# Optimization experiments

Hardware: AMD Instinct MI355X
Metric: run time of the kernel (lower is better)

Reference implementation:

```python
import jax, jax.numpy as jnp
import numpy as np

N = 50000   # nodes
E = 800000  # edges
D = 128     # input feature dim
H = 128     # hidden dim
L = 3       # num GIN layers
G = 64      # graphs in batch


def setup_inputs() -> dict:
    key = jax.random.key(0)
    ks = jax.random.split(key, 20)
    inp = {
        "h": jax.random.normal(ks[0], (N, D), jnp.float32),
        "src": jax.random.randint(ks[1], (E,), 0, N),
        "dst": jax.random.randint(ks[2], (E,), 0, N),
        "graph_ids": jnp.sort(jax.random.randint(ks[3], (N,), 0, G)),
    }
    k = 4
    for i in range(L):
        in_dim = D if i == 0 else H
        inp[f"w1_{i}"] = jax.random.normal(ks[k], (in_dim, H), jnp.float32) / np.sqrt(in_dim).astype(np.float32); k += 1
        inp[f"b1_{i}"] = jnp.zeros((H,), jnp.float32)
        inp[f"w2_{i}"] = jax.random.normal(ks[k], (H, H), jnp.float32) / np.sqrt(H).astype(np.float32); k += 1
        inp[f"b2_{i}"] = jnp.zeros((H,), jnp.float32)
    inp["w_out"] = jax.random.normal(ks[k], (H * L, 1), jnp.float32) / np.sqrt(H * L).astype(np.float32)
    inp["b_out"] = jnp.zeros((1,), jnp.float32)
    return inp


def _gin_layer(h, src, dst, w1, b1, w2, b2):
    # sum aggregation over edges: agg[i] = sum_{(j->i) in E} h[j]
    agg = jax.ops.segment_sum(h[src], dst, num_segments=N)
    z = h + agg  # (1 + eps) * h + agg with eps = 0 (DGL GINConv default)
    return jax.nn.relu(z @ w1 + b1) @ w2 + b2  # 2-layer MLP


def reference(h, src, dst, graph_ids,
              w1_0, b1_0, w2_0, b2_0,
              w1_1, b1_1, w2_1, b2_1,
              w1_2, b1_2, w2_2, b2_2,
              w_out, b_out):
    layers = [(w1_0, b1_0, w2_0, b2_0),
              (w1_1, b1_1, w2_1, b2_1),
              (w1_2, b1_2, w2_2, b2_2)]
    readouts = []
    for w1, b1, w2, b2 in layers:
        h = _gin_layer(h, src, dst, w1, b1, w2, b2)
        # per-graph sum readout of node features: [G, H]
        readouts.append(jax.ops.segment_sum(h, graph_ids, num_segments=G))
    hg = jnp.concatenate(readouts, axis=1)  # [G, H*L]
    return hg @ w_out + b_out  # [G, 1]
```

## Files before the change

kernel.cpp:

```cpp
#include <hip/hip_runtime.h>

#define NN 50000
#define NE 800000
#define DIMH 128
#define NGRAPH 64
#define NTILES 3125
#define MLP_BLOCKS 1563
#define NBIN 196
#define BCAP 8064
#define SL_US 800000
#define SL_U4 100000

typedef __attribute__((ext_vector_type(8))) short bf16x8;
typedef __attribute__((ext_vector_type(4))) float f32x4;

__device__ __forceinline__ unsigned short f2b(float f) {
  unsigned int b = __float_as_uint(f);
  unsigned int r = (b + 0x7FFFu + ((b >> 16) & 1u)) >> 16;
  return (unsigned short)r;
}
__device__ __forceinline__ float b2f_lo(unsigned int u) { return __uint_as_float(u << 16); }
__device__ __forceinline__ float b2f_hi(unsigned int u) { return __uint_as_float(u & 0xffff0000u); }
__device__ __forceinline__ unsigned int pk2(float lo, float hi) {
  return (unsigned int)f2b(lo) | ((unsigned int)f2b(hi) << 16);
}
__device__ __forceinline__ void add8(float* a, uint4 u) {
  a[0] += b2f_lo(u.x); a[1] += b2f_hi(u.x);
  a[2] += b2f_lo(u.y); a[3] += b2f_hi(u.y);
  a[4] += b2f_lo(u.z); a[5] += b2f_hi(u.z);
  a[6] += b2f_lo(u.w); a[7] += b2f_hi(u.w);
}


__global__ __launch_bounds__(256) void bin_scatter_kernel(const int* __restrict__ src,
                                                          const int* __restrict__ dst,
                                                          int* __restrict__ gcnt,
                                                          int2* __restrict__ staging) {
  __shared__ int hist[NBIN];
  __shared__ int base[NBIN];
  int tid = threadIdx.x;
  for (int i = tid; i < NBIN; i += 256) hist[i] = 0;
  __syncthreads();
  int e0 = blockIdx.x * 2048;
  int2 ed[8];
  int bin[8], rank[8];
#pragma unroll
  for (int k = 0; k < 8; ++k) {
    int e = e0 + k * 256 + tid;
    bin[k] = 0; rank[k] = 0; ed[k] = make_int2(0, 0);
    if (e < NE) {
      ed[k].x = src[e]; ed[k].y = dst[e];
      bin[k] = ed[k].y >> 8;
      rank[k] = atomicAdd(&hist[bin[k]], 1);
    }
  }
  __syncthreads();
  for (int i = tid; i < NBIN; i += 256) base[i] = atomicAdd(&gcnt[i], hist[i]);
  __syncthreads();
#pragma unroll
  for (int k = 0; k < 8; ++k) {
    int e = e0 + k * 256 + tid;
    if (e < NE) staging[bin[k] * BCAP + base[bin[k]] + rank[k]] = ed[k];
  }
}

__global__ __launch_bounds__(256) void bin_fill_kernel(const int2* __restrict__ staging,
                                                       const int* __restrict__ gcnt,
                                                       int* __restrict__ adj,
                                                       int* __restrict__ row_ptr,
                                                       int* __restrict__ cnt,
                                                       int* __restrict__ alloc) {
  __shared__ int hdeg[256], loc[256], c2[256];
  __shared__ int sbase;
  int b = blockIdx.x;
  int tid = threadIdx.x;
  hdeg[tid] = 0; c2[tid] = 0;
  __syncthreads();
  int n = gcnt[b];
  for (int i = tid; i < n; i += 256)
    atomicAdd(&hdeg[staging[b * BCAP + i].y & 255], 1);
  __syncthreads();
  int v = hdeg[tid];
  int va = (v + 1) & ~1;
  loc[tid] = va;
  __syncthreads();
  for (int off = 1; off < 256; off <<= 1) {
    int t = (tid >= off) ? loc[tid - off] : 0;
    __syncthreads();
    loc[tid] += t;
    __syncthreads();
  }
  if (tid == 255) sbase = atomicAdd(alloc, loc[255]);
  __syncthreads();
  int excl = loc[tid] - va;
  int node = b * 256 + tid;
  if (node < NN) { row_ptr[node] = sbase + excl; cnt[node] = v; }
  loc[tid] = excl;
  __syncthreads();
  for (int i = tid; i < n; i += 256) {
    int2 e = staging[b * BCAP + i];
    int local = e.y & 255;
    int r = atomicAdd(&c2[local], 1);
    adj[sbase + loc[local] + r] = e.x;
  }
}


struct WPtrs { const float* w[6]; const float* b_out; const float* b2_last;
               const float* w_out; };

__global__ __launch_bounds__(256) void prep_kernel(WPtrs ptrs, unsigned short* __restrict__ wt,
                                                   float* __restrict__ out,
                                                   int* __restrict__ gcnt,
                                                   int* __restrict__ alloc,
                                                   float* __restrict__ v2,
                                                   float* __restrict__ s2) {
  int i = blockIdx.x * 256 + threadIdx.x;
  int m = i >> 14;
  int idx = i & 16383;
  int c = idx >> 7, k = idx & 127;
  wt[m * 16384 + idx] = f2b(ptrs.w[m][k * DIMH + c]);
  if (i < NGRAPH) out[i] = ptrs.b_out[0];
  if (i < NBIN) gcnt[i] = 0;
  if (i == NBIN) *alloc = 0;
  if (i < DIMH) {
    const float* w2r = ptrs.w[5] + i * DIMH;
    const float* wo = ptrs.w_out + 2 * DIMH;
    float s0 = 0.f, s1 = 0.f, sa = 0.f, sb = 0.f;
#pragma unroll 4
    for (int cc = 0; cc < DIMH; cc += 4) {
      s0 += w2r[cc] * wo[cc];
      s1 += w2r[cc + 1] * wo[cc + 1];
      sa += w2r[cc + 2] * wo[cc + 2];
      sb += w2r[cc + 3] * wo[cc + 3];
    }
    v2[i] = (s0 + s1) + (sa + sb);
  }
  if (i == DIMH) {
    const float* wo = ptrs.w_out + 2 * DIMH;
    float s0 = 0.f, s1 = 0.f, sa = 0.f, sb = 0.f;
#pragma unroll 4
    for (int cc = 0; cc < DIMH; cc += 4) {
      s0 += ptrs.b2_last[cc] * wo[cc];
      s1 += ptrs.b2_last[cc + 1] * wo[cc + 1];
      sa += ptrs.b2_last[cc + 2] * wo[cc + 2];
      sb += ptrs.b2_last[cc + 3] * wo[cc + 3];
    }
    *s2 = (s0 + s1) + (sa + sb);
  }
}

__global__ void convh_kernel(const float* __restrict__ h, uint2* __restrict__ Hs) {
  int t = blockIdx.x * 256 + threadIdx.x;
  if (t >= NN * 32) return;
  int node = t >> 5;
  int q = t & 31;
  float4 v = *(const float4*)&h[node * DIMH + q * 4];
  uint2 o;
  o.x = pk2(v.x, v.y);
  o.y = pk2(v.z, v.w);
  Hs[(q >> 2) * (SL_U4 * 2) + node * 4 + (q & 3)] = o;
}

__global__ __launch_bounds__(256) void agg_kernel(const uint4* __restrict__ Hs,
                                                  const int* __restrict__ row_ptr,
                                                  const int* __restrict__ cnt,
                                                  const int* __restrict__ adj,
                                                  uint4* __restrict__ Zs) {
  int bid = blockIdx.x;
  int slice = bid & 7;
  int nb = bid >> 3;
  int tid = threadIdx.x;
  int node = nb * 128 + (tid >> 1);
  int l2 = tid & 1;
  if (node >= NN) return;
  const uint4* hp = Hs + slice * SL_U4;
  int start = row_ptr[node];
  int c = cnt[node];
  float a[8];
  {
    uint4 own = hp[node * 2 + l2];
    a[0] = b2f_lo(own.x); a[1] = b2f_hi(own.x);
    a[2] = b2f_lo(own.y); a[3] = b2f_hi(own.y);
    a[4] = b2f_lo(own.z); a[5] = b2f_hi(own.z);
    a[6] = b2f_lo(own.w); a[7] = b2f_hi(own.w);
  }
  int j = 0;
  for (; j + 8 <= c; j += 8) {
    int2 i01 = *(const int2*)(adj + start + j);
    int2 i23 = *(const int2*)(adj + start + j + 2);
    int2 i45 = *(const int2*)(adj + start + j + 4);
    int2 i67 = *(const int2*)(adj + start + j + 6);
    uint4 u0 = hp[i01.x * 2 + l2];
    uint4 u1 = hp[i01.y * 2 + l2];
    uint4 u2 = hp[i23.x * 2 + l2];
    uint4 u3 = hp[i23.y * 2 + l2];
    uint4 u4 = hp[i45.x * 2 + l2];
    uint4 u5 = hp[i45.y * 2 + l2];
    uint4 u6 = hp[i67.x * 2 + l2];
    uint4 u7 = hp[i67.y * 2 + l2];
    add8(a, u0); add8(a, u1); add8(a, u2); add8(a, u3);
    add8(a, u4); add8(a, u5); add8(a, u6); add8(a, u7);
  }
  for (; j + 2 <= c; j += 2) {
    int2 i01 = *(const int2*)(adj + start + j);
    uint4 u0 = hp[i01.x * 2 + l2];
    uint4 u1 = hp[i01.y * 2 + l2];
    add8(a, u0); add8(a, u1);
  }
  if (j < c) {
    int n0 = adj[start + j];
    add8(a, hp[n0 * 2 + l2]);
  }
  uint4 o;
  o.x = pk2(a[0], a[1]);
  o.y = pk2(a[2], a[3]);
  o.z = pk2(a[4], a[5]);
  o.w = pk2(a[6], a[7]);
  Zs[slice * SL_U4 + node * 2 + l2] = o;
}

__global__ __launch_bounds__(256, 4) void mlp_kernel(const unsigned short* __restrict__ X,
                                                     const unsigned short* __restrict__ W1t,
                                                     const float* __restrict__ b1,
                                                     const unsigned short* __restrict__ W2t,
                                                     const float* __restrict__ b2,
                                                     unsigned short* __restrict__ Y,
                                                     const int* __restrict__ gids,
                                                     const float* __restrict__ wout,
                                                     float* __restrict__ gout,
                                                     const float* __restrict__ v2,
                                                     const float* __restrict__ s2p) {
  __shared__ unsigned short y1[2][2048];
  __shared__ float s_gout[NGRAPH];
  int tid = threadIdx.x;
  if (tid < NGRAPH) s_gout[tid] = 0.f;
  bool last = (v2 != nullptr);

  int wv = tid >> 6;
  int lane = tid & 63;
  int pb = wv >> 1;
  int half = wv & 1;
  int l15 = lane & 15;
  int g = lane >> 4;
  int rtc = blockIdx.x * 2 + pb;
  bool active = rtc < NTILES;
  int rts = active ? rtc : 0;

  int asl_base = (g >> 1) * SL_US + (g & 1) * 8 + l15 * 16;
  bf16x8 a[4];
  {
    int roff = rts * 256;
#pragma unroll
    for (int kt = 0; kt < 4; ++kt)
      a[kt] = *(const bf16x8*)(X + 2 * kt * SL_US + roff + asl_base);
  }

  bf16x8 fb1[4][4];
  const unsigned short* w1b = W1t + (half * 64 + l15) * DIMH + g * 8;
#pragma unroll
  for (int n = 0; n < 4; ++n)
#pragma unroll
    for (int kt = 0; kt < 4; ++kt)
      fb1[n][kt] = *(const bf16x8*)(w1b + n * 16 * DIMH + kt * 32);

  float b1v[4], v2v[4];
#pragma unroll
  for (int n = 0; n < 4; ++n) {
    int col = half * 64 + n * 16 + l15;
    b1v[n] = b1[col];
    v2v[n] = last ? v2[col] : 0.f;
  }
  float s2v = last ? *s2p : 0.f;
  __syncthreads();

  unsigned short* buf = y1[pb];
  if (active) {
    float pr1[4] = {0.f, 0.f, 0.f, 0.f};
#pragma unroll
    for (int n = 0; n < 4; ++n) {
      f32x4 acc = (f32x4){0.f, 0.f, 0.f, 0.f};
#pragma unroll
      for (int kt = 0; kt < 4; ++kt)
        acc = __builtin_amdgcn_mfma_f32_16x16x32_bf16(a[kt], fb1[n][kt], acc, 0, 0, 0);
      int col2 = (half * 64 + n * 16 + l15) * 2;
#pragma unroll
      for (int r = 0; r < 4; ++r) {
        float f = fmaxf(acc[r] + b1v[n], 0.f);
        if (!last) {
          int row = 4 * g + r;
          buf[((row * 256 + col2) ^ (row << 4)) >> 1] = f2b(f);
        } else {
          pr1[r] += f * v2v[n];
        }
      }
    }
    if (last) {
#pragma unroll
      for (int r = 0; r < 4; ++r) {
#pragma unroll
        for (int off = 1; off < 16; off <<= 1) pr1[r] += __shfl_xor(pr1[r], off, 64);
      }
      if (l15 == 0) {
        float s2add = (half == 0) ? s2v : 0.f;
#pragma unroll
        for (int r = 0; r < 4; ++r)
          atomicAdd(&s_gout[gids[rtc * 16 + 4 * g + r]], pr1[r] + s2add);
      }
    }
  }

  if (!last) {
    bf16x8 fb2[4][4];
    const unsigned short* w2b = W2t + (half * 64 + l15) * DIMH + g * 8;
#pragma unroll
    for (int n = 0; n < 4; ++n)
#pragma unroll
      for (int kt = 0; kt < 4; ++kt)
        fb2[n][kt] = *(const bf16x8*)(w2b + n * 16 * DIMH + kt * 32);
    float b2v[4], wov[4];
#pragma unroll
    for (int n = 0; n < 4; ++n) {
      int col = half * 64 + n * 16 + l15;
      b2v[n] = b2[col];
      wov[n] = wout[col];
    }

    __syncthreads();

    if (active) {
      bf16x8 a2[4];
#pragma unroll
      for (int kt = 0; kt < 4; ++kt)
        a2[kt] = *(const bf16x8*)&buf[((l15 * 256 + kt * 64 + g * 16) ^ (l15 << 4)) >> 1];

      float pr[4] = {0.f, 0.f, 0.f, 0.f};
#pragma unroll
      for (int n = 0; n < 4; ++n) {
        f32x4 acc = (f32x4){0.f, 0.f, 0.f, 0.f};
#pragma unroll
        for (int kt = 0; kt < 4; ++kt)
          acc = __builtin_amdgcn_mfma_f32_16x16x32_bf16(a2[kt], fb2[n][kt], acc, 0, 0, 0);
        int sl = 4 * half + n;
#pragma unroll
        for (int r = 0; r < 4; ++r) {
          float f = acc[r] + b2v[n];
          Y[sl * SL_US + (rtc * 16 + 4 * g + r) * 16 + l15] = f2b(f);
          pr[r] += f * wov[n];
        }
      }
#pragma unroll
      for (int r = 0; r < 4; ++r) {
#pragma unroll
        for (int off = 1; off < 16; off <<= 1) pr[r] += __shfl_xor(pr[r], off, 64);
      }
      if (l15 == 0) {
#pragma unroll
        for (int r = 0; r < 4; ++r)
          atomicAdd(&s_gout[gids[rtc * 16 + 4 * g + r]], pr[r]);
      }
    }
  }

  __syncthreads();
  if (tid < NGRAPH) {
    float v = s_gout[tid];
    if (v != 0.f) atomicAdd(&gout[tid], v);
  }
}


extern "C" void kernel_launch(void* const* d_in, const int* in_sizes, int n_in,
                              void* d_out, int out_size, void* d_ws, size_t ws_size,
                              hipStream_t stream) {
  const float* h = (const float*)d_in[0];
  const int* src = (const int*)d_in[1];
  const int* dst = (const int*)d_in[2];
  const int* gids = (const int*)d_in[3];
  const float* w_out = (const float*)d_in[16];
  const float* b_out = (const float*)d_in[17];
  float* out = (float*)d_out;

  char* base = (char*)d_ws;
  unsigned short* buf0 = (unsigned short*)(base);
  unsigned short* buf1 = (unsigned short*)(base + 12800000);
  int2* staging = (int2*)(base + 25600000);
  int* adj = (int*)(base + 38400000);
  int* row_ptr = (int*)(base + 41800064);
  int* cnt = (int*)(base + 42000128);
  int* gcnt = (int*)(base + 42200192);
  int* alloc = (int*)(base + 42201024);
  unsigned short* wt = (unsigned short*)(base + 42201088);
  float* v2 = (float*)(base + 42397696);
  float* s2 = (float*)(base + 42398208);
  unsigned short* Zs = (unsigned short*)(base + 42400000);

  WPtrs ptrs;
  for (int l = 0; l < 3; ++l) {
    ptrs.w[2 * l] = (const float*)d_in[4 + l * 4];
    ptrs.w[2 * l + 1] = (const float*)d_in[6 + l * 4];
  }
  ptrs.b_out = b_out;
  ptrs.b2_last = (const float*)d_in[15];
  ptrs.w_out = w_out;

  prep_kernel<<<384, 256, 0, stream>>>(ptrs, wt, out, gcnt, alloc, v2, s2);
  bin_scatter_kernel<<<(NE + 2047) / 2048, 256, 0, stream>>>(src, dst, gcnt, staging);
  bin_fill_kernel<<<NBIN, 256, 0, stream>>>(staging, gcnt, adj, row_ptr, cnt, alloc);
  convh_kernel<<<(NN * 32 + 255) / 256, 256, 0, stream>>>(h, (uint2*)buf0);

  int agg_blocks = 391 * 8;

  for (int l = 0; l < 3; ++l) {
    const float* b1 = (const float*)d_in[5 + l * 4];
    const float* b2 = (const float*)d_in[7 + l * 4];
    const unsigned short* Hl = (l & 1) ? buf1 : buf0;
    unsigned short* Yl = (l & 1) ? buf0 : buf1;
    int lastl = (l == 2);
    agg_kernel<<<agg_blocks, 256, 0, stream>>>((const uint4*)Hl, row_ptr, cnt, adj,
                                               (uint4*)Zs);
    mlp_kernel<<<MLP_BLOCKS, 256, 0, stream>>>(Zs, wt + (2 * l) * 16384, b1,
                                               wt + (2 * l + 1) * 16384, b2,
                                               lastl ? nullptr : Yl,
                                               gids, w_out + l * DIMH, out,
                                               lastl ? v2 : nullptr,
                                               lastl ? s2 : nullptr);
  }
}
```

Measured before the change: 237.0 us.

## Make MLP kernels persistent with weight reuse and next-tile prefetch

```diff
diff --git a/kernel.cpp b/kernel.cpp
--- a/kernel.cpp
+++ b/kernel.cpp
@@ -5,7 +5,9 @@
 #define DIMH 128
 #define NGRAPH 64
 #define NTILES 3125
-#define MLP_BLOCKS 1563
+#define PAIRS 1024
+#define MLP_BLOCKS 512
+#define MLP_ITERS 4
 #define NBIN 196
 #define BCAP 8064
 #define SL_US 800000
@@ -220,22 +222,19 @@
   Zs[slice * SL_U4 + node * 2 + l2] = o;
 }
 
-__global__ __launch_bounds__(256, 4) void mlp_kernel(const unsigned short* __restrict__ X,
-                                                     const unsigned short* __restrict__ W1t,
-                                                     const float* __restrict__ b1,
-                                                     const unsigned short* __restrict__ W2t,
-                                                     const float* __restrict__ b2,
-                                                     unsigned short* __restrict__ Y,
-                                                     const int* __restrict__ gids,
-                                                     const float* __restrict__ wout,
-                                                     float* __restrict__ gout,
-                                                     const float* __restrict__ v2,
-                                                     const float* __restrict__ s2p) {
-  __shared__ unsigned short y1[2][2048];
+__global__ __launch_bounds__(256, 2) void mlp_mid_kernel(const unsigned short* __restrict__ X,
+                                                         const unsigned short* __restrict__ W1t,
+                                                         const float* __restrict__ b1,
+                                                         const unsigned short* __restrict__ W2t,
+                                                         const float* __restrict__ b2,
+                                                         unsigned short* __restrict__ Y,
+                                                         const int* __restrict__ gids,
+                                                         const float* __restrict__ wout,
+                                                         float* __restrict__ gout) {
+  __shared__ unsigned short y1[2][2][2048];
   __shared__ float s_gout[NGRAPH];
   int tid = threadIdx.x;
   if (tid < NGRAPH) s_gout[tid] = 0.f;
-  bool last = (v2 != nullptr);
 
   int wv = tid >> 6;
   int lane = tid & 63;
@@ -243,87 +242,67 @@
   int half = wv & 1;
   int l15 = lane & 15;
   int g = lane >> 4;
-  int rtc = blockIdx.x * 2 + pb;
-  bool active = rtc < NTILES;
-  int rts = active ? rtc : 0;
+  int p = blockIdx.x * 2 + pb;
 
   int asl_base = (g >> 1) * SL_US + (g & 1) * 8 + l15 * 16;
+
   bf16x8 a[4];
   {
-    int roff = rts * 256;
+    int roff = p * 256;
 #pragma unroll
     for (int kt = 0; kt < 4; ++kt)
       a[kt] = *(const bf16x8*)(X + 2 * kt * SL_US + roff + asl_base);
   }
 
-  bf16x8 fb1[4][4];
+  bf16x8 fb1[4][4], fb2[4][4];
   const unsigned short* w1b = W1t + (half * 64 + l15) * DIMH + g * 8;
+  const unsigned short* w2b = W2t + (half * 64 + l15) * DIMH + g * 8;
 #pragma unroll
   for (int n = 0; n < 4; ++n)
 #pragma unroll
-    for (int kt = 0; kt < 4; ++kt)
+    for (int kt = 0; kt < 4; ++kt) {
       fb1[n][kt] = *(const bf16x8*)(w1b + n * 16 * DIMH + kt * 32);
-
-  float b1v[4], v2v[4];
+      fb2[n][kt] = *(const bf16x8*)(w2b + n * 16 * DIMH + kt * 32);
+    }
+  float b1v[4], b2v[4], wov[4];
 #pragma unroll
   for (int n = 0; n < 4; ++n) {
     int col = half * 64 + n * 16 + l15;
     b1v[n] = b1[col];
-    v2v[n] = last ? v2[col] : 0.f;
-  }
-  float s2v = last ? *s2p : 0.f;
-  __syncthreads();
-
-  unsigned short* buf = y1[pb];
-  if (active) {
-    float pr1[4] = {0.f, 0.f, 0.f, 0.f};
-#pragma unroll
-    for (int n = 0; n < 4; ++n) {
-      f32x4 acc = (f32x4){0.f, 0.f, 0.f, 0.f};
-#pragma unroll
-      for (int kt = 0; kt < 4; ++kt)
-        acc = __builtin_amdgcn_mfma_f32_16x16x32_bf16(a[kt], fb1[n][kt], acc, 0, 0, 0);
-      int col2 = (half * 64 + n * 16 + l15) * 2;
-#pragma unroll
-      for (int r = 0; r < 4; ++r) {
-        float f = fmaxf(acc[r] + b1v[n], 0.f);
-        if (!last) {
+    b2v[n] = b2[col];
+    wov[n] = wout[col];
+  }
+  __syncthreads();
+
+#pragma unroll
+  for (int i = 0; i < MLP_ITERS; ++i) {
+    int rtc = p + i * PAIRS;
+    bool active = rtc < NTILES;
+    unsigned short* buf = y1[pb][i & 1];
+
+    if (active) {
+#pragma unroll
+      for (int n = 0; n < 4; ++n) {
+        f32x4 acc = (f32x4){0.f, 0.f, 0.f, 0.f};
+#pragma unroll
+        for (int kt = 0; kt < 4; ++kt)
+          acc = __builtin_amdgcn_mfma_f32_16x16x32_bf16(a[kt], fb1[n][kt], acc, 0, 0, 0);
+        int col2 = (half * 64 + n * 16 + l15) * 2;
+#pragma unroll
+        for (int r = 0; r < 4; ++r) {
+          float f = fmaxf(acc[r] + b1v[n], 0.f);
           int row = 4 * g + r;
           buf[((row * 256 + col2) ^ (row << 4)) >> 1] = f2b(f);
-        } else {
-          pr1[r] += f * v2v[n];
         }
       }
     }
-    if (last) {
-#pragma unroll
-      for (int r = 0; r < 4; ++r) {
-#pragma unroll
-        for (int off = 1; off < 16; off <<= 1) pr1[r] += __shfl_xor(pr1[r], off, 64);
-      }
-      if (l15 == 0) {
-        float s2add = (half == 0) ? s2v : 0.f;
-#pragma unroll
-        for (int r = 0; r < 4; ++r)
-          atomicAdd(&s_gout[gids[rtc * 16 + 4 * g + r]], pr1[r] + s2add);
-      }
-    }
-  }
-
-  if (!last) {
-    bf16x8 fb2[4][4];
-    const unsigned short* w2b = W2t + (half * 64 + l15) * DIMH + g * 8;
-#pragma unroll
-    for (int n = 0; n < 4; ++n)
+
+    int rtn = p + (i + 1) * PAIRS;
+    if (i + 1 < MLP_ITERS && rtn < NTILES) {
+      int roff = rtn * 256;
 #pragma unroll
       for (int kt = 0; kt < 4; ++kt)
-        fb2[n][kt] = *(const bf16x8*)(w2b + n * 16 * DIMH + kt * 32);
-    float b2v[4], wov[4];
-#pragma unroll
-    for (int n = 0; n < 4; ++n) {
-      int col = half * 64 + n * 16 + l15;
-      b2v[n] = b2[col];
-      wov[n] = wout[col];
+        a[kt] = *(const bf16x8*)(X + 2 * kt * SL_US + roff + asl_base);
     }
 
     __syncthreads();
@@ -358,6 +337,100 @@
 #pragma unroll
         for (int r = 0; r < 4; ++r)
           atomicAdd(&s_gout[gids[rtc * 16 + 4 * g + r]], pr[r]);
+      }
+    }
+  }
+
+  __syncthreads();
+  if (tid < NGRAPH) {
+    float v = s_gout[tid];
+    if (v != 0.f) atomicAdd(&gout[tid], v);
+  }
+}
+
+__global__ __launch_bounds__(256, 2) void mlp_last_kernel(const unsigned short* __restrict__ X,
+                                                          const unsigned short* __restrict__ W1t,
+                                                          const float* __restrict__ b1,
+                                                          const int* __restrict__ gids,
+                                                          float* __restrict__ gout,
+                                                          const float* __restrict__ v2,
+                                                          const float* __restrict__ s2p) {
+  __shared__ float s_gout[NGRAPH];
+  int tid = threadIdx.x;
+  if (tid < NGRAPH) s_gout[tid] = 0.f;
+
+  int wv = tid >> 6;
+  int lane = tid & 63;
+  int half = wv & 1;
+  int pbase = blockIdx.x * 2 + (wv >> 1);
+  int l15 = lane & 15;
+  int g = lane >> 4;
+
+  int asl_base = (g >> 1) * SL_US + (g & 1) * 8 + l15 * 16;
+
+  bf16x8 fb1[4][4];
+  const unsigned short* w1b = W1t + (half * 64 + l15) * DIMH + g * 8;
+#pragma unroll
+  for (int n = 0; n < 4; ++n)
+#pragma unroll
+    for (int kt = 0; kt < 4; ++kt)
+      fb1[n][kt] = *(const bf16x8*)(w1b + n * 16 * DIMH + kt * 32);
+  float b1v[4], v2v[4];
+#pragma unroll
+  for (int n = 0; n < 4; ++n) {
+    int col = half * 64 + n * 16 + l15;
+    b1v[n] = b1[col];
+    v2v[n] = v2[col];
+  }
+  float s2v = (half == 0) ? *s2p : 0.f;
+  __syncthreads();
+
+  bf16x8 a[4];
+  {
+    int roff = pbase * 256;
+#pragma unroll
+    for (int kt = 0; kt < 4; ++kt)
+      a[kt] = *(const bf16x8*)(X + 2 * kt * SL_US + roff + asl_base);
+  }
+
+#pragma unroll
+  for (int i = 0; i < MLP_ITERS; ++i) {
+    int rtc = pbase + i * PAIRS;
+    bool active = rtc < NTILES;
+
+    bf16x8 cur[4];
+#pragma unroll
+    for (int kt = 0; kt < 4; ++kt) cur[kt] = a[kt];
+
+    int rtn = pbase + (i + 1) * PAIRS;
+    if (i + 1 < MLP_ITERS && rtn < NTILES) {
+      int roff = rtn * 256;
+#pragma unroll
+      for (int kt = 0; kt < 4; ++kt)
+        a[kt] = *(const bf16x8*)(X + 2 * kt * SL_US + roff + asl_base);
+    }
+
+    if (active) {
+      float pr[4] = {0.f, 0.f, 0.f, 0.f};
+#pragma unroll
+      for (int n = 0; n < 4; ++n) {
+        f32x4 acc = (f32x4){0.f, 0.f, 0.f, 0.f};
+#pragma unroll
+        for (int kt = 0; kt < 4; ++kt)
+          acc = __builtin_amdgcn_mfma_f32_16x16x32_bf16(cur[kt], fb1[n][kt], acc, 0, 0, 0);
+#pragma unroll
+        for (int r = 0; r < 4; ++r)
+          pr[r] += fmaxf(acc[r] + b1v[n], 0.f) * v2v[n];
+      }
+#pragma unroll
+      for (int r = 0; r < 4; ++r) {
+#pragma unroll
+        for (int off = 1; off < 16; off <<= 1) pr[r] += __shfl_xor(pr[r], off, 64);
+      }
+      if (l15 == 0) {
+#pragma unroll
+        for (int r = 0; r < 4; ++r)
+          atomicAdd(&s_gout[gids[rtc * 16 + 4 * g + r]], pr[r] + s2v);
       }
     }
   }
@@ -416,14 +489,15 @@
     const float* b2 = (const float*)d_in[7 + l * 4];
     const unsigned short* Hl = (l & 1) ? buf1 : buf0;
     unsigned short* Yl = (l & 1) ? buf0 : buf1;
-    int lastl = (l == 2);
     agg_kernel<<<agg_blocks, 256, 0, stream>>>((const uint4*)Hl, row_ptr, cnt, adj,
                                                (uint4*)Zs);
-    mlp_kernel<<<MLP_BLOCKS, 256, 0, stream>>>(Zs, wt + (2 * l) * 16384, b1,
-                                               wt + (2 * l + 1) * 16384, b2,
-                                               lastl ? nullptr : Yl,
-                                               gids, w_out + l * DIMH, out,
-                                               lastl ? v2 : nullptr,
-                                               lastl ? s2 : nullptr);
-  }
-}
+    if (l < 2) {
+      mlp_mid_kernel<<<MLP_BLOCKS, 256, 0, stream>>>(Zs, wt + (2 * l) * 16384, b1,
+                                                     wt + (2 * l + 1) * 16384, b2,
+                                                     Yl, gids, w_out + l * DIMH, out);
+    } else {
+      mlp_last_kernel<<<MLP_BLOCKS, 256, 0, stream>>>(Zs, wt + (2 * l) * 16384, b1,
+                                                      gids, out, v2, s2);
+    }
+  }
+}
```

After: 215.2 us. -9.2%, faster.
